# Kernel optimization log

Measured on AMD Instinct MI355X. Metric: run time of the kernel, lower is better.

Reference implementation:

```python
import jax, jax.numpy as jnp
import numpy as np

L_LAYERS, N_TRACES, N_THETA = 250, 600, 30


def setup_inputs() -> dict:
    key = jax.random.key(0)
    k1, k2, k3, k4, k5 = jax.random.split(key, 5)
    # physically plausible elastic parameters (keeps asin args inside (-1,1))
    vp = 2500.0 + 1500.0 * jax.random.uniform(k1, (L_LAYERS, N_TRACES), dtype=jnp.float32)
    vs = vp * (0.45 + 0.1 * jax.random.uniform(k2, (L_LAYERS, N_TRACES), dtype=jnp.float32))
    rho = 2.2 + 0.4 * jax.random.uniform(k3, (L_LAYERS, N_TRACES), dtype=jnp.float32)
    # incidence angles in radians, up to ~31.5 degrees
    theta = jnp.sort(0.05 + 0.5 * jax.random.uniform(k4, (N_THETA,), dtype=jnp.float32))
    wavemat = 0.1 * jax.random.normal(k5, (L_LAYERS, L_LAYERS), dtype=jnp.float32)
    return {"vp": vp, "vs": vs, "rho": rho, "theta": theta, "wavemat": wavemat}


def reference(vp, vs, rho, theta, wavemat):
    # vp/vs/rho: [L, T]; theta: [A]; wavemat: [L, L]
    L, T = vp.shape
    A = theta.shape[0]
    # interface properties: upper (1) / lower (2) layer, shape [L-1, T, 1]
    a1, a2 = vp[:-1, :, None], vp[1:, :, None]
    b1, b2 = vs[:-1, :, None], vs[1:, :, None]
    r1, r2 = rho[:-1, :, None], rho[1:, :, None]
    th = theta[None, None, :]                      # [1, 1, A]
    p = jnp.sin(th) / a1                           # ray parameter, [L-1, T, A]
    shp = p.shape
    theta2 = jnp.arcsin(jnp.clip(p * a2, -1.0, 1.0))
    phi1 = jnp.arcsin(jnp.clip(p * b1, -1.0, 1.0))
    phi2 = jnp.arcsin(jnp.clip(p * b2, -1.0, 1.0))
    sth = jnp.broadcast_to(jnp.sin(th), shp)
    cth = jnp.broadcast_to(jnp.cos(th), shp)
    sth2, cth2 = jnp.sin(theta2), jnp.cos(theta2)
    sp1, cp1 = jnp.sin(phi1), jnp.cos(phi1)
    sp2, cp2 = jnp.sin(phi2), jnp.cos(phi2)
    q1 = r1 * b1 * (1.0 - 2.0 * sp1 ** 2)          # shear impedance terms
    q2 = r2 * b2 * (1.0 - 2.0 * sp2 ** 2)
    row_m2 = jnp.stack([2.0 * r1 * b1 * sp1 * cth, q1, 2.0 * r2 * b2 * sp2 * cth2, q2], axis=-1)
    # M, N: [L-1, T, A, 4, 4]
    M = jnp.stack([
        jnp.stack([-sth, -cp1, sth2, cp2], axis=-1),
        jnp.stack([cth, -sp1, cth2, -sp2], axis=-1),
        row_m2,
        jnp.stack([-r1 * a1 * (1.0 - 2.0 * sp1 ** 2), r1 * b1 * jnp.sin(2.0 * phi1),
                   r2 * a2 * (1.0 - 2.0 * sp2 ** 2), -r2 * b2 * jnp.sin(2.0 * phi2)], axis=-1),
    ], axis=-2)
    N = jnp.stack([
        jnp.stack([sth, cp1, -sth2, -cp2], axis=-1),
        jnp.stack([cth, -sp1, cth2, -sp2], axis=-1),
        row_m2,
        jnp.stack([r1 * a1 * (1.0 - 2.0 * sp1 ** 2), -r1 * b1 * jnp.sin(2.0 * phi1),
                   -r2 * a2 * (1.0 - 2.0 * sp2 ** 2), r2 * b2 * jnp.sin(2.0 * phi2)], axis=-1),
    ], axis=-2)
    # PdPu = (inv(M) @ N)[0, 0] == solve(M, N[:, 0])[0]
    rpp = jnp.linalg.solve(M, N[..., :, 0:1])[..., 0, 0]   # [L-1, T, A]
    ref = jnp.zeros((T, L, A), dtype=vp.dtype)
    ref = ref.at[:, : L - 1, :].set(jnp.moveaxis(rpp, 1, 0))
    # convolve with wavelet matrix per trace: [L, L] @ [T, L, A]
    cal_data = jnp.einsum('lk,tka->tla', wavemat, ref)
    return cal_data
```

## Files before the change

kernel.cpp:

```cpp
#include <hip/hip_runtime.h>

constexpr int L  = 250;
constexpr int T  = 600;
constexpr int A  = 30;

typedef _Float16 h8  __attribute__((ext_vector_type(8)));
typedef float    f4  __attribute__((ext_vector_type(4)));

constexpr int RT_LD = 264;

__global__ __launch_bounds__(256)
void wm_to_h(const float* __restrict__ wm, _Float16* __restrict__ wmh)
{
    const int m = blockIdx.x;
    const int k = threadIdx.x;
    _Float16 v = (_Float16)0.0f;
    if (m < L && k < L) v = (_Float16)wm[m * L + k];
    wmh[m * 256 + k] = v;
}

__global__ __launch_bounds__(256)
void zoep_fused(const float* __restrict__ vp,
                const float* __restrict__ vs,
                const float* __restrict__ rho,
                const float* __restrict__ theta,
                const _Float16* __restrict__ wmh,
                float* __restrict__ out)
{
    __shared__ _Float16 refT[32 * RT_LD];
    __shared__ float sth_s[32];
    __shared__ float cth_s[32];

    const int tid = threadIdx.x;
    const int t   = blockIdx.x;

    if (tid < 32) {
        const float th = (tid < A) ? theta[tid] : 0.0f;
        sth_s[tid] = sinf(th);
        cth_s[tid] = cosf(th);
    }
    __syncthreads();

    const int aq = tid & 7;
    const int a0 = aq << 2;
    const int kb = tid >> 3;

    for (int g = 0; g < 8; ++g) {
        const int k = g * 32 + kb;
        float res[4] = {0.f, 0.f, 0.f, 0.f};

        if (k < L - 1) {
            const float a1 = vp[k * T + t];
            const float a2 = vp[(k + 1) * T + t];
            const float b1 = vs[k * T + t];
            const float b2 = vs[(k + 1) * T + t];
            const float r1 = rho[k * T + t];
            const float r2 = rho[(k + 1) * T + t];

            const float ra1  = __builtin_amdgcn_rcpf(a1);
            const float rb1  = r1 * b1, rb2 = r2 * b2;
            const float ra1r = r1 * a1, ra2r = r2 * a2;

#pragma unroll
            for (int j = 0; j < 4; ++j) {
                const float sth = sth_s[a0 + j];
                const float cth = cth_s[a0 + j];

                const float p   = sth * ra1;
                const float s2  = p * a2;
                const float c2  = sqrtf(1.0f - s2 * s2);
                const float sp1 = p * b1;
                const float cp1 = sqrtf(1.0f - sp1 * sp1);
                const float sp2 = p * b2;
                const float cp2 = sqrtf(1.0f - sp2 * sp2);

                const float k1 = 1.0f - 2.0f * sp1 * sp1;
                const float k2 = 1.0f - 2.0f * sp2 * sp2;
                const float q1 = rb1 * k1;
                const float q2 = rb2 * k2;
                const float P1 = ra1r * k1;
                const float P2 = ra2r * k2;
                const float u1 = 2.0f * rb1 * sp1;
                const float u2 = 2.0f * rb2 * sp2;
                const float S1 = u1 * cp1;
                const float S2 = u2 * cp2;
                const float g1 = u1 * cth;
                const float g2 = u2 * c2;

                const float m00 = -sth, m01 = -cp1, m02 = s2,  m03 = cp2;
                const float m10 =  cth, m11 = -sp1, m12 = c2,  m13 = -sp2;
                const float m20 =  g1,  m21 =  q1,  m22 = g2,  m23 = q2;
                const float m30 = -P1,  m31 =  S1,  m32 = P2,  m33 = -S2;

                const float s3v = m01 * m12 - m11 * m02;
                const float s4v = m01 * m13 - m11 * m03;
                const float s5v = m02 * m13 - m12 * m03;
                const float c3v = m21 * m32 - m31 * m22;
                const float c4v = m21 * m33 - m31 * m23;
                const float c5v = m22 * m33 - m32 * m23;
                const float s0v = m00 * m11 - m10 * m01;
                const float s1v = m00 * m12 - m10 * m02;
                const float s2v = m00 * m13 - m10 * m03;
                const float c0v = m20 * m31 - m30 * m21;
                const float c1v = m20 * m32 - m30 * m22;
                const float c2v = m20 * m33 - m30 * m23;

                const float detM = s0v*c5v - s1v*c4v + s2v*c3v
                                 + s3v*c2v - s4v*c1v + s5v*c0v;
                const float A0 = m11*c5v - m12*c4v + m13*c3v;
                const float A3 = m21*s5v - m22*s4v + m23*s3v;

                const float num = m00 * A0 - m30 * A3;
                res[j] = 1.0f - 2.0f * num * __builtin_amdgcn_rcpf(detM);
            }
            if (aq == 7) { res[2] = 0.0f; res[3] = 0.0f; }
        }
#pragma unroll
        for (int j = 0; j < 4; ++j)
            refT[(a0 + j) * RT_LD + k] = (_Float16)res[j];
    }
    __syncthreads();

    const int w    = tid >> 6;
    const int lane = tid & 63;
    const int quad = lane >> 4;
    const int n16  = lane & 15;

    f4 acc[4][2];
#pragma unroll
    for (int mi = 0; mi < 4; ++mi)
#pragma unroll
        for (int nt = 0; nt < 2; ++nt) acc[mi][nt] = (f4){0.f, 0.f, 0.f, 0.f};

#pragma unroll
    for (int ks = 0; ks < 8; ++ks) {
        const int kofs = ks * 32 + quad * 8;
        const h8 b0 = *(const h8*)&refT[ n16       * RT_LD + kofs];
        const h8 b1 = *(const h8*)&refT[(16 + n16) * RT_LD + kofs];
#pragma unroll
        for (int mi = 0; mi < 4; ++mi) {
            const int m = (w * 4 + mi) * 16 + n16;
            const h8 af = *(const h8*)&wmh[m * 256 + kofs];
            acc[mi][0] = __builtin_amdgcn_mfma_f32_16x16x32_f16(af, b0, acc[mi][0], 0, 0, 0);
            acc[mi][1] = __builtin_amdgcn_mfma_f32_16x16x32_f16(af, b1, acc[mi][1], 0, 0, 0);
        }
    }

    float* outt = out + (size_t)t * (L * A);
#pragma unroll
    for (int mi = 0; mi < 4; ++mi) {
        const int mbase = (w * 4 + mi) * 16 + quad * 4;
#pragma unroll
        for (int nt = 0; nt < 2; ++nt) {
            const int a = nt * 16 + n16;
            if (a < A) {
#pragma unroll
                for (int r = 0; r < 4; ++r) {
                    const int l = mbase + r;
                    if (l < L) outt[l * A + a] = acc[mi][nt][r];
                }
            }
        }
    }
}

extern "C" void kernel_launch(void* const* d_in, const int* in_sizes, int n_in,
                              void* d_out, int out_size, void* d_ws, size_t ws_size,
                              hipStream_t stream) {
    (void)in_sizes; (void)n_in; (void)out_size; (void)ws_size;
    const float* vp    = (const float*)d_in[0];
    const float* vs    = (const float*)d_in[1];
    const float* rho   = (const float*)d_in[2];
    const float* theta = (const float*)d_in[3];
    const float* wm    = (const float*)d_in[4];
    float* out = (float*)d_out;
    _Float16* wmh = (_Float16*)d_ws;

    wm_to_h<<<dim3(256), dim3(256), 0, stream>>>(wm, wmh);
    zoep_fused<<<dim3(T), dim3(256), 0, stream>>>(vp, vs, rho, theta, wmh, out);
}
```

Measured before the change: 100.9 us.

## Fuse wavelet fp16 conversion into main kernel and map one interface per thread

Drops the separate kernel that converted the wavelet matrix to fp16 in the workspace. The main kernel now reads fp32 rows directly and converts them on the fly, with clamped and masked loads at the edges. The Zoeppritz stage is also remapped so each thread handles one interface across all 30 angles, loading the six layer properties once instead of eight times per thread. This removes one launch and the redundant global loads, at the cost of more global traffic and conversion work inside the MFMA loop, repeated in every block.

```diff
diff --git a/kernel.cpp b/kernel.cpp
--- a/kernel.cpp
+++ b/kernel.cpp
@@ -10,21 +10,11 @@
 constexpr int RT_LD = 264;
 
 __global__ __launch_bounds__(256)
-void wm_to_h(const float* __restrict__ wm, _Float16* __restrict__ wmh)
-{
-    const int m = blockIdx.x;
-    const int k = threadIdx.x;
-    _Float16 v = (_Float16)0.0f;
-    if (m < L && k < L) v = (_Float16)wm[m * L + k];
-    wmh[m * 256 + k] = v;
-}
-
-__global__ __launch_bounds__(256)
 void zoep_fused(const float* __restrict__ vp,
                 const float* __restrict__ vs,
                 const float* __restrict__ rho,
                 const float* __restrict__ theta,
-                const _Float16* __restrict__ wmh,
+                const float* __restrict__ wm,
                 float* __restrict__ out)
 {
     __shared__ _Float16 refT[32 * RT_LD];
@@ -41,84 +31,77 @@
     }
     __syncthreads();
 
-    const int aq = tid & 7;
-    const int a0 = aq << 2;
-    const int kb = tid >> 3;
+    const int  k     = tid;
+    const bool valid = (k < L - 1);
+    const int  kc    = valid ? k : (L - 2);
 
-    for (int g = 0; g < 8; ++g) {
-        const int k = g * 32 + kb;
-        float res[4] = {0.f, 0.f, 0.f, 0.f};
+    const float a1 = vp[kc * T + t];
+    const float a2 = vp[(kc + 1) * T + t];
+    const float b1 = vs[kc * T + t];
+    const float b2 = vs[(kc + 1) * T + t];
+    const float r1 = rho[kc * T + t];
+    const float r2 = rho[(kc + 1) * T + t];
 
-        if (k < L - 1) {
-            const float a1 = vp[k * T + t];
-            const float a2 = vp[(k + 1) * T + t];
-            const float b1 = vs[k * T + t];
-            const float b2 = vs[(k + 1) * T + t];
-            const float r1 = rho[k * T + t];
-            const float r2 = rho[(k + 1) * T + t];
+    const float ra1  = __builtin_amdgcn_rcpf(a1);
+    const float rb1  = r1 * b1, rb2 = r2 * b2;
+    const float ra1r = r1 * a1, ra2r = r2 * a2;
 
-            const float ra1  = __builtin_amdgcn_rcpf(a1);
-            const float rb1  = r1 * b1, rb2 = r2 * b2;
-            const float ra1r = r1 * a1, ra2r = r2 * a2;
+#pragma unroll 2
+    for (int a = 0; a < A; ++a) {
+        const float sth = sth_s[a];
+        const float cth = cth_s[a];
 
-#pragma unroll
-            for (int j = 0; j < 4; ++j) {
-                const float sth = sth_s[a0 + j];
-                const float cth = cth_s[a0 + j];
+        const float p   = sth * ra1;
+        const float s2  = p * a2;
+        const float c2  = sqrtf(1.0f - s2 * s2);
+        const float sp1 = p * b1;
+        const float cp1 = sqrtf(1.0f - sp1 * sp1);
+        const float sp2 = p * b2;
+        const float cp2 = sqrtf(1.0f - sp2 * sp2);
 
-                const float p   = sth * ra1;
-                const float s2  = p * a2;
-                const float c2  = sqrtf(1.0f - s2 * s2);
-                const float sp1 = p * b1;
-                const float cp1 = sqrtf(1.0f - sp1 * sp1);
-                const float sp2 = p * b2;
-                const float cp2 = sqrtf(1.0f - sp2 * sp2);
+        const float k1 = 1.0f - 2.0f * sp1 * sp1;
+        const float k2 = 1.0f - 2.0f * sp2 * sp2;
+        const float q1 = rb1 * k1;
+        const float q2 = rb2 * k2;
+        const float P1 = ra1r * k1;
+        const float P2 = ra2r * k2;
+        const float u1 = 2.0f * rb1 * sp1;
+        const float u2 = 2.0f * rb2 * sp2;
+        const float S1 = u1 * cp1;
+        const float S2 = u2 * cp2;
+        const float g1 = u1 * cth;
+        const float g2 = u2 * c2;
 
-                const float k1 = 1.0f - 2.0f * sp1 * sp1;
-                const float k2 = 1.0f - 2.0f * sp2 * sp2;
-                const float q1 = rb1 * k1;
-                const float q2 = rb2 * k2;
-                const float P1 = ra1r * k1;
-                const float P2 = ra2r * k2;
-                const float u1 = 2.0f * rb1 * sp1;
-                const float u2 = 2.0f * rb2 * sp2;
-                const float S1 = u1 * cp1;
-                const float S2 = u2 * cp2;
-                const float g1 = u1 * cth;
-                const float g2 = u2 * c2;
+        const float m00 = -sth, m01 = -cp1, m02 = s2,  m03 = cp2;
+        const float m10 =  cth, m11 = -sp1, m12 = c2,  m13 = -sp2;
+        const float m20 =  g1,  m21 =  q1,  m22 = g2,  m23 = q2;
+        const float m30 = -P1,  m31 =  S1,  m32 = P2,  m33 = -S2;
 
-                const float m00 = -sth, m01 = -cp1, m02 = s2,  m03 = cp2;
-                const float m10 =  cth, m11 = -sp1, m12 = c2,  m13 = -sp2;
-                const float m20 =  g1,  m21 =  q1,  m22 = g2,  m23 = q2;
-                const float m30 = -P1,  m31 =  S1,  m32 = P2,  m33 = -S2;
+        const float s3v = m01 * m12 - m11 * m02;
+        const float s4v = m01 * m13 - m11 * m03;
+        const float s5v = m02 * m13 - m12 * m03;
+        const float c3v = m21 * m32 - m31 * m22;
+        const float c4v = m21 * m33 - m31 * m23;
+        const float c5v = m22 * m33 - m32 * m23;
+        const float s0v = m00 * m11 - m10 * m01;
+        const float s1v = m00 * m12 - m10 * m02;
+        const float s2v = m00 * m13 - m10 * m03;
+        const float c0v = m20 * m31 - m30 * m21;
+        const float c1v = m20 * m32 - m30 * m22;
+        const float c2v = m20 * m33 - m30 * m23;
 
-                const float s3v = m01 * m12 - m11 * m02;
-                const float s4v = m01 * m13 - m11 * m03;
-                const float s5v = m02 * m13 - m12 * m03;
-                const float c3v = m21 * m32 - m31 * m22;
-                const float c4v = m21 * m33 - m31 * m23;
-                const float c5v = m22 * m33 - m32 * m23;
-                const float s0v = m00 * m11 - m10 * m01;
-                const float s1v = m00 * m12 - m10 * m02;
-                const float s2v = m00 * m13 - m10 * m03;
-                const float c0v = m20 * m31 - m30 * m21;
-                const float c1v = m20 * m32 - m30 * m22;
-                const float c2v = m20 * m33 - m30 * m23;
+        const float detM = s0v*c5v - s1v*c4v + s2v*c3v
+                         + s3v*c2v - s4v*c1v + s5v*c0v;
+        const float A0 = m11*c5v - m12*c4v + m13*c3v;
+        const float A3 = m21*s5v - m22*s4v + m23*s3v;
 
-                const float detM = s0v*c5v - s1v*c4v + s2v*c3v
-                                 + s3v*c2v - s4v*c1v + s5v*c0v;
-                const float A0 = m11*c5v - m12*c4v + m13*c3v;
-                const float A3 = m21*s5v - m22*s4v + m23*s3v;
+        const float num = m00 * A0 - m30 * A3;
+        const float res = 1.0f - 2.0f * num * __builtin_amdgcn_rcpf(detM);
 
-                const float num = m00 * A0 - m30 * A3;
-                res[j] = 1.0f - 2.0f * num * __builtin_amdgcn_rcpf(detM);
-            }
-            if (aq == 7) { res[2] = 0.0f; res[3] = 0.0f; }
-        }
-#pragma unroll
-        for (int j = 0; j < 4; ++j)
-            refT[(a0 + j) * RT_LD + k] = (_Float16)res[j];
+        refT[a * RT_LD + k] = (_Float16)(valid ? res : 0.0f);
     }
+    refT[30 * RT_LD + k] = (_Float16)0.0f;
+    refT[31 * RT_LD + k] = (_Float16)0.0f;
     __syncthreads();
 
     const int w    = tid >> 6;
@@ -139,8 +122,20 @@
         const h8 b1 = *(const h8*)&refT[(16 + n16) * RT_LD + kofs];
 #pragma unroll
         for (int mi = 0; mi < 4; ++mi) {
-            const int m = (w * 4 + mi) * 16 + n16;
-            const h8 af = *(const h8*)&wmh[m * 256 + kofs];
+            const int m    = (w * 4 + mi) * 16 + n16;
+            const int rowc = (m < L) ? m : (L - 1);
+            const float* wrow = wm + rowc * L;
+
+            h8 af;
+#pragma unroll
+            for (int c = 0; c < 4; ++c) {
+                const int col  = kofs + 2 * c;
+                const int colc = (col <= L - 2) ? col : (L - 2);
+                const float2 f = *(const float2*)(wrow + colc);
+                af[2 * c]     = (_Float16)((col     < L) ? f.x : 0.0f);
+                af[2 * c + 1] = (_Float16)((col + 1 < L) ? f.y : 0.0f);
+            }
+
             acc[mi][0] = __builtin_amdgcn_mfma_f32_16x16x32_f16(af, b0, acc[mi][0], 0, 0, 0);
             acc[mi][1] = __builtin_amdgcn_mfma_f32_16x16x32_f16(af, b1, acc[mi][1], 0, 0, 0);
         }
@@ -167,15 +162,13 @@
 extern "C" void kernel_launch(void* const* d_in, const int* in_sizes, int n_in,
                               void* d_out, int out_size, void* d_ws, size_t ws_size,
                               hipStream_t stream) {
-    (void)in_sizes; (void)n_in; (void)out_size; (void)ws_size;
+    (void)in_sizes; (void)n_in; (void)out_size; (void)d_ws; (void)ws_size;
     const float* vp    = (const float*)d_in[0];
     const float* vs    = (const float*)d_in[1];
     const float* rho   = (const float*)d_in[2];
     const float* theta = (const float*)d_in[3];
     const float* wm    = (const float*)d_in[4];
     float* out = (float*)d_out;
-    _Float16* wmh = (_Float16*)d_ws;
 
-    wm_to_h<<<dim3(256), dim3(256), 0, stream>>>(wm, wmh);
-    zoep_fused<<<dim3(T), dim3(256), 0, stream>>>(vp, vs, rho, theta, wmh, out);
+    zoep_fused<<<dim3(T), dim3(256), 0, stream>>>(vp, vs, rho, theta, wm, out);
 }
```

New measurement: 99.91 us, median of 3. Within noise of the previous version (-1.0%).
